# Kernel tuning notes

Hardware: AMD Instinct MI355X
Metric: run time of the kernel (lower is better)

Reference implementation:

```python
import jax, jax.numpy as jnp
import numpy as np

LAM = 0.1       # self.lam
MAX_ITER = 100  # fista_reweighted maxIter
TOL = 1e-5      # convergence tolerance


def creat_dictionary(T, rr, theta):
    # torch creatRealDictionary: row i = [1, rr^i*cos(i*theta), rr^i*sin(i*theta)]
    i = jnp.arange(T, dtype=rr.dtype)[:, None]           # [T,1]
    p = rr[None, :] ** i                                  # [T,P]
    W1 = p * jnp.cos(i * theta[None, :])                  # [T,P]
    W2 = p * jnp.sin(i * theta[None, :])                  # [T,P]
    ones = jnp.ones((T, 1), rr.dtype)
    return jnp.concatenate([ones, W1, W2], axis=1)        # [T, 1+2P]


def fista_reweighted(D, Y, lambd, w):
    # D: [T,K], Y: [N,T,M], w: [N,K,M]
    DtD = D.T @ D                                         # [K,K]
    DtY = jnp.einsum('tk,ntm->nkm', D, Y)                 # [N,K,M]
    # torch.norm(DtD, 2) with no dim = 2-norm of the flattened matrix (Frobenius)
    Linv = 1.0 / jnp.linalg.norm(DtD)
    K = DtD.shape[0]
    A = jnp.eye(K, dtype=D.dtype) - DtD * Linv            # [K,K]
    wl = w * (lambd * Linv)                               # weighted lambda [N,K,M]
    c_minus = DtY * Linv - wl
    c_plus = DtY * Linv + wl
    x0 = jnp.zeros_like(DtY)

    def body(carry, _):
        x_old, y_old, t_old, done = carry
        Ay = jnp.einsum('kj,njm->nkm', A, y_old)
        # shrinkage: max(0, Ay + c-) + min(0, Ay + c+)
        x_new = jnp.maximum(0.0, Ay + c_minus) + jnp.minimum(0.0, Ay + c_plus)
        t_new = (1.0 + jnp.sqrt(1.0 + 4.0 * t_old ** 2)) / 2.0
        tt = (t_old - 1.0) / t_new
        y_new = x_new + tt * (x_new - x_old)
        conv = (jnp.linalg.norm(x_old - x_new) / K) < TOL
        stop = done | conv
        # on convergence torch breaks with x_old = x_new; afterwards freeze state
        x_next = jnp.where(done, x_old, x_new)
        y_next = jnp.where(stop, y_old, y_new)
        t_next = jnp.where(stop, t_old, t_new)
        return (x_next, y_next, t_next, stop), None

    init = (x0, x0, jnp.float32(1.0), jnp.array(False))
    (x, _, _, _), _ = jax.lax.scan(jax.checkpoint(body), init, None, length=MAX_ITER)
    return x


def setup_inputs() -> dict:
    key = jax.random.key(0)
    k1, k2, k3 = jax.random.split(key, 3)
    N, T, M, P = 256, 36, 50, 80
    x = jax.random.normal(k1, (N, T, M), dtype=jnp.float32)
    rr = 0.9 + 0.1 * jax.random.uniform(k2, (P,), dtype=jnp.float32)   # poles near unit circle
    theta = jnp.pi * jax.random.uniform(k3, (P,), dtype=jnp.float32)
    return {"x": x, "rr": rr, "theta": theta, "T": T}


def reference(x, rr, theta, T):
    dic = creat_dictionary(T, rr, theta)                  # [T,K]
    K = dic.shape[1]
    w = jnp.ones((x.shape[0], K, x.shape[2]), x.dtype)    # [N,K,M]
    code = None
    for _ in range(2):                                    # reweighting heuristic, 2 passes
        code = fista_reweighted(dic, x, LAM, w)
        wn = 1.0 / (jnp.abs(code) + 0.01)
        w = wn / jnp.linalg.norm(wn) * K
    reconst = jnp.einsum('tk,nkm->ntm', dic, code)        # [N,T,M]
    return code, dic, reconst
```

## Files before the change

kernel.cpp:

```cpp
#include <hip/hip_runtime.h>
#include <math.h>

#define N_    256
#define T_    36
#define M_    50
#define P_    80
#define K_    161
#define PADK  192
#define KC    24
#define NB    200
#define NT    256
#define LAM_  0.1f
#define MAXIT 100

#define KM_     (K_*M_)
#define TM_     (T_*M_)
#define OUT_DIC 2060800
#define OUT_REC 2066596

#define WS_LINV 0
#define WS_D    64
#define WS_ACC  8192
#define WS_WN   8392
#define WS_BARC 8396
#define WS_BARG 8397

__global__ __launch_bounds__(256) void k_dict(const float* __restrict__ rr,
                                              const float* __restrict__ th,
                                              float* __restrict__ out,
                                              float* __restrict__ ws) {
    __shared__ float Dl[T_*PADK];
    const int tid = threadIdx.x;
    for (int e = tid; e < T_*PADK; e += 256) {
        int t = e / PADK, k = e - (e / PADK) * PADK;
        float v = 0.f;
        if (k == 0) v = 1.f;
        else if (k <= P_)      { float r = rr[k-1];     float a = th[k-1]*(float)t;
                                 v = powf(r, (float)t) * cosf(a); }
        else if (k <= 2*P_)    { float r = rr[k-1-P_];  float a = th[k-1-P_]*(float)t;
                                 v = powf(r, (float)t) * sinf(a); }
        Dl[e] = v;
        ws[WS_D + e] = v;
        if (k < K_) out[OUT_DIC + t*K_ + k] = v;
    }
    __syncthreads();
    float loc = 0.f;
    for (int e = tid; e < T_*T_; e += 256) {
        int t1 = e / T_, t2 = e - (e / T_) * T_;
        float s = 0.f;
        for (int k = 0; k < K_; ++k) s = fmaf(Dl[t1*PADK+k], Dl[t2*PADK+k], s);
        loc = fmaf(s, s, loc);
    }
    #pragma unroll
    for (int mm = 1; mm < 64; mm <<= 1) loc += __shfl_xor(loc, mm);
    __shared__ float rb[4];
    if ((tid & 63) == 0) rb[tid >> 6] = loc;
    __syncthreads();
    if (tid == 0) {
        float tot = rb[0] + rb[1] + rb[2] + rb[3];
        ws[WS_LINV] = 1.0f / sqrtf(tot);
    }
}

__device__ __forceinline__ void grid_barrier(unsigned* cnt, unsigned* gen) {
    __syncthreads();
    if (threadIdx.x == 0) {
        __threadfence();
        unsigned g0 = __hip_atomic_load(gen, __ATOMIC_ACQUIRE, __HIP_MEMORY_SCOPE_AGENT);
        unsigned my = __hip_atomic_fetch_add(cnt, 1u, __ATOMIC_ACQ_REL, __HIP_MEMORY_SCOPE_AGENT);
        if (my == NB - 1u) {
            __hip_atomic_store(cnt, 0u, __ATOMIC_RELAXED, __HIP_MEMORY_SCOPE_AGENT);
            __hip_atomic_fetch_add(gen, 1u, __ATOMIC_RELEASE, __HIP_MEMORY_SCOPE_AGENT);
        } else {
            while (__hip_atomic_load(gen, __ATOMIC_ACQUIRE, __HIP_MEMORY_SCOPE_AGENT) == g0)
                __builtin_amdgcn_s_sleep(1);
        }
        __threadfence();
    }
    __syncthreads();
}

template<int CTRL>
__device__ __forceinline__ float dpp_mov(float v) {
    int p = __builtin_amdgcn_update_dpp(0, __float_as_int(v), CTRL, 0xF, 0xF, true);
    return __int_as_float(p);
}
__device__ __forceinline__ float reduce8(float z) {
    z += dpp_mov<0xB1>(z);
    z += dpp_mov<0x4E>(z);
    z += dpp_mov<0x141>(z);
    return z;
}

__global__ __launch_bounds__(NT, 1) void k_fista(const float* __restrict__ X,
                                                 float* __restrict__ out,
                                                 float* __restrict__ ws) {
    __shared__ __align__(16) float Dl[T_*PADK];
    __shared__ int   sniter;
    __shared__ float sbcast;

    unsigned* wsu = (unsigned*)ws;
    const int tid = threadIdx.x;

    for (int e = tid; e < T_*PADK; e += NT) Dl[e] = ws[WS_D + e];
    const float Linv = ws[WS_LINV];
    __syncthreads();

    const int lane  = tid & 63;
    const int kq    = lane & 7;
    const int gw    = (int)blockIdx.x * (NT/64) + (tid >> 6);
    const int colb  = gw*16 + (lane >> 3)*2;
    const int n0    = colb / M_;
    const int m0    = colb - n0*M_;
    const int n1    = (colb+1) / M_;
    const int m1    = (colb+1) - n1*M_;
    const int kbase = kq * KC;
    const float* Y0 = X + n0*TM_ + m0;
    const float* Y1 = X + n1*TM_ + m1;

    float x[2][KC], y[2][KC], b[2][KC], wl[2][KC];

    #pragma unroll
    for (int j = 0; j < KC; ++j) { b[0][j] = 0.f; b[1][j] = 0.f; }
    #pragma unroll 2
    for (int t = 0; t < T_; ++t) {
        float yv0 = Y0[t*M_], yv1 = Y1[t*M_];
        const float4* dp = (const float4*)(Dl + t*PADK + kbase);
        #pragma unroll
        for (int q = 0; q < KC/4; ++q) {
            float4 d = dp[q];
            b[0][4*q+0] = fmaf(d.x, yv0, b[0][4*q+0]);
            b[0][4*q+1] = fmaf(d.y, yv0, b[0][4*q+1]);
            b[0][4*q+2] = fmaf(d.z, yv0, b[0][4*q+2]);
            b[0][4*q+3] = fmaf(d.w, yv0, b[0][4*q+3]);
            b[1][4*q+0] = fmaf(d.x, yv1, b[1][4*q+0]);
            b[1][4*q+1] = fmaf(d.y, yv1, b[1][4*q+1]);
            b[1][4*q+2] = fmaf(d.z, yv1, b[1][4*q+2]);
            b[1][4*q+3] = fmaf(d.w, yv1, b[1][4*q+3]);
        }
    }
    #pragma unroll
    for (int j = 0; j < KC; ++j) { b[0][j] *= Linv; b[1][j] *= Linv; }

    #pragma unroll
    for (int j = 0; j < KC; ++j) { wl[0][j] = LAM_ * Linv; wl[1][j] = LAM_ * Linv; }

    float tcur = 1.f;

    auto iterate = [&]() -> float {
        float u[2][KC];
        #pragma unroll
        for (int j = 0; j < KC; ++j) { u[0][j] = 0.f; u[1][j] = 0.f; }
        #pragma unroll 2
        for (int t = 0; t < T_; ++t) {
            const float4* dp = (const float4*)(Dl + t*PADK + kbase);
            float4 da[KC/4];
            #pragma unroll
            for (int q = 0; q < KC/4; ++q) da[q] = dp[q];
            float z00=0.f, z01=0.f, z02=0.f, z03=0.f;
            float z10=0.f, z11=0.f, z12=0.f, z13=0.f;
            #pragma unroll
            for (int q = 0; q < KC/4; ++q) {
                z00 = fmaf(da[q].x, y[0][4*q+0], z00);
                z01 = fmaf(da[q].y, y[0][4*q+1], z01);
                z02 = fmaf(da[q].z, y[0][4*q+2], z02);
                z03 = fmaf(da[q].w, y[0][4*q+3], z03);
                z10 = fmaf(da[q].x, y[1][4*q+0], z10);
                z11 = fmaf(da[q].y, y[1][4*q+1], z11);
                z12 = fmaf(da[q].z, y[1][4*q+2], z12);
                z13 = fmaf(da[q].w, y[1][4*q+3], z13);
            }
            float z0 = (z00+z01) + (z02+z03);
            float z1 = (z10+z11) + (z12+z13);
            z0 = reduce8(z0);
            z1 = reduce8(z1);
            #pragma unroll
            for (int q = 0; q < KC/4; ++q) {
                u[0][4*q+0] = fmaf(da[q].x, z0, u[0][4*q+0]);
                u[0][4*q+1] = fmaf(da[q].y, z0, u[0][4*q+1]);
                u[0][4*q+2] = fmaf(da[q].z, z0, u[0][4*q+2]);
                u[0][4*q+3] = fmaf(da[q].w, z0, u[0][4*q+3]);
                u[1][4*q+0] = fmaf(da[q].x, z1, u[1][4*q+0]);
                u[1][4*q+1] = fmaf(da[q].y, z1, u[1][4*q+1]);
                u[1][4*q+2] = fmaf(da[q].z, z1, u[1][4*q+2]);
                u[1][4*q+3] = fmaf(da[q].w, z1, u[1][4*q+3]);
            }
        }
        float t0 = tcur;
        float t1 = 0.5f * (1.f + sqrtf(fmaf(4.f*t0, t0, 1.f)));
        float tt = (t0 - 1.f) / t1;
        tcur = t1;
        float ss = 0.f;
        #pragma unroll
        for (int c = 0; c < 2; ++c) {
            #pragma unroll
            for (int j = 0; j < KC; ++j) {
                float Ay = fmaf(-Linv, u[c][j], y[c][j]);
                float s  = Ay + b[c][j];
                float xn = fmaxf(0.f, s - wl[c][j]) + fminf(0.f, s + wl[c][j]);
                float d  = xn - x[c][j];
                ss    = fmaf(d, d, ss);
                y[c][j] = fmaf(tt, d, xn);
                x[c][j] = xn;
            }
        }
        return ss;
    };

    auto run = [&](int nit, bool record, int accbase) {
        tcur = 1.f;
        #pragma unroll
        for (int j = 0; j < KC; ++j) {
            x[0][j] = 0.f; x[1][j] = 0.f; y[0][j] = 0.f; y[1][j] = 0.f;
        }
        for (int i = 0; i < nit; ++i) {
            float ss = iterate();
            if (record) {
                #pragma unroll
                for (int mm = 1; mm < 64; mm <<= 1) ss += __shfl_xor(ss, mm);
                if (lane == 0) atomicAdd(ws + WS_ACC + accbase + i, ss);
            }
        }
    };

    const float THR2 = (1e-5f * (float)K_) * (1e-5f * (float)K_);

    #pragma unroll 1
    for (int pass = 0; pass < 2; ++pass) {
        run(MAXIT, true, pass*MAXIT);
        grid_barrier(wsu + WS_BARC, wsu + WS_BARG);

        if (tid == 0) sniter = MAXIT + 1;
        __syncthreads();
        if (tid < MAXIT) {
            float a = __hip_atomic_load(ws + WS_ACC + pass*MAXIT + tid,
                                        __ATOMIC_RELAXED, __HIP_MEMORY_SCOPE_AGENT);
            if (a < THR2) atomicMin(&sniter, tid + 1);
        }
        __syncthreads();
        int nit2 = sniter;
        if (nit2 < MAXIT) run(nit2, false, 0);

        if (pass == 0) {
            float loc = 0.f;
            #pragma unroll
            for (int c = 0; c < 2; ++c) {
                #pragma unroll
                for (int j = 0; j < KC; ++j) {
                    float wn = 1.0f / (fabsf(x[c][j]) + 0.01f);
                    wl[c][j] = wn;
                    if (kbase + j < K_) loc = fmaf(wn, wn, loc);
                }
            }
            #pragma unroll
            for (int mm = 1; mm < 64; mm <<= 1) loc += __shfl_xor(loc, mm);
            if (lane == 0) atomicAdd(ws + WS_WN, loc);
            grid_barrier(wsu + WS_BARC, wsu + WS_BARG);
            if (tid == 0)
                sbcast = __hip_atomic_load(ws + WS_WN, __ATOMIC_RELAXED,
                                           __HIP_MEMORY_SCOPE_AGENT);
            __syncthreads();
            float scale = ((float)K_) * (LAM_ * Linv) / sqrtf(sbcast);
            #pragma unroll
            for (int j = 0; j < KC; ++j) { wl[0][j] *= scale; wl[1][j] *= scale; }
        }
    }

    #pragma unroll
    for (int j = 0; j < KC; ++j) {
        int kg = kbase + j;
        if (kg < K_) {
            out[n0*KM_ + kg*M_ + m0] = x[0][j];
            out[n1*KM_ + kg*M_ + m1] = x[1][j];
        }
    }
    #pragma unroll 2
    for (int t = 0; t < T_; ++t) {
        const float4* dp = (const float4*)(Dl + t*PADK + kbase);
        float z00=0.f, z01=0.f, z02=0.f, z03=0.f;
        float z10=0.f, z11=0.f, z12=0.f, z13=0.f;
        #pragma unroll
        for (int q = 0; q < KC/4; ++q) {
            float4 d = dp[q];
            z00 = fmaf(d.x, x[0][4*q+0], z00);
            z01 = fmaf(d.y, x[0][4*q+1], z01);
            z02 = fmaf(d.z, x[0][4*q+2], z02);
            z03 = fmaf(d.w, x[0][4*q+3], z03);
            z10 = fmaf(d.x, x[1][4*q+0], z10);
            z11 = fmaf(d.y, x[1][4*q+1], z11);
            z12 = fmaf(d.z, x[1][4*q+2], z12);
            z13 = fmaf(d.w, x[1][4*q+3], z13);
        }
        float z0 = (z00+z01) + (z02+z03);
        float z1 = (z10+z11) + (z12+z13);
        z0 = reduce8(z0);
        z1 = reduce8(z1);
        if (kq == (t & 7)) {
            out[OUT_REC + n0*TM_ + t*M_ + m0] = z0;
            out[OUT_REC + n1*TM_ + t*M_ + m1] = z1;
        }
    }
}

extern "C" void kernel_launch(void* const* d_in, const int* in_sizes, int n_in,
                              void* d_out, int out_size, void* d_ws, size_t ws_size,
                              hipStream_t stream) {
    const float* X  = (const float*)d_in[0];
    const float* rr = (const float*)d_in[1];
    const float* th = (const float*)d_in[2];
    float* out = (float*)d_out;
    float* ws  = (float*)d_ws;

    hipMemsetAsync((char*)d_ws + WS_ACC*sizeof(float), 0, 4096, stream);
    k_dict<<<dim3(1), dim3(256), 0, stream>>>(rr, th, out, ws);
    k_fista<<<dim3(NB), dim3(NT), 0, stream>>>(X, out, ws);
}
```

Baseline: 1.889 ms.

## Split K across 16 lanes with 512-thread blocks and cache dictionary rows in registers

Each column pair is now handled by 16 lanes holding 12 coefficients each instead of 8 lanes holding 24, with blocks doubled to 512 threads. The DPP reduction gains a fourth step to cover 16 lanes. The first 6 dictionary rows for each lane's slice are preloaded into registers so those rows skip shared-memory loads every iteration. This raises thread-level parallelism and cuts per-thread register state, at the cost of a longer reduction, more lanes touching shared memory, and more cross-block barrier participants.

```diff
diff --git a/kernel.cpp b/kernel.cpp
--- a/kernel.cpp
+++ b/kernel.cpp
@@ -7,9 +7,10 @@
 #define P_    80
 #define K_    161
 #define PADK  192
-#define KC    24
+#define KC    12
+#define NC    6
 #define NB    200
-#define NT    256
+#define NT    512
 #define LAM_  0.1f
 #define MAXIT 100
 
@@ -85,14 +86,15 @@
     int p = __builtin_amdgcn_update_dpp(0, __float_as_int(v), CTRL, 0xF, 0xF, true);
     return __int_as_float(p);
 }
-__device__ __forceinline__ float reduce8(float z) {
+__device__ __forceinline__ float reduce16(float z) {
     z += dpp_mov<0xB1>(z);
     z += dpp_mov<0x4E>(z);
     z += dpp_mov<0x141>(z);
+    z += dpp_mov<0x140>(z);
     return z;
 }
 
-__global__ __launch_bounds__(NT, 1) void k_fista(const float* __restrict__ X,
+__global__ __launch_bounds__(NT, 2) void k_fista(const float* __restrict__ X,
                                                  float* __restrict__ out,
                                                  float* __restrict__ ws) {
     __shared__ __align__(16) float Dl[T_*PADK];
@@ -107,16 +109,23 @@
     __syncthreads();
 
     const int lane  = tid & 63;
-    const int kq    = lane & 7;
+    const int sub   = lane & 15;
     const int gw    = (int)blockIdx.x * (NT/64) + (tid >> 6);
-    const int colb  = gw*16 + (lane >> 3)*2;
+    const int colb  = gw*8 + (lane >> 4)*2;
     const int n0    = colb / M_;
     const int m0    = colb - n0*M_;
     const int n1    = (colb+1) / M_;
     const int m1    = (colb+1) - n1*M_;
-    const int kbase = kq * KC;
+    const int kbase = sub * KC;
     const float* Y0 = X + n0*TM_ + m0;
     const float* Y1 = X + n1*TM_ + m1;
+
+    float4 dc[NC*3];
+    #pragma unroll
+    for (int t = 0; t < NC; ++t) {
+        const float4* dp = (const float4*)(Dl + t*PADK + kbase);
+        dc[t*3+0] = dp[0]; dc[t*3+1] = dp[1]; dc[t*3+2] = dp[2];
+    }
 
     float x[2][KC], y[2][KC], b[2][KC], wl[2][KC];
 
@@ -151,16 +160,13 @@
         float u[2][KC];
         #pragma unroll
         for (int j = 0; j < KC; ++j) { u[0][j] = 0.f; u[1][j] = 0.f; }
-        #pragma unroll 2
-        for (int t = 0; t < T_; ++t) {
-            const float4* dp = (const float4*)(Dl + t*PADK + kbase);
-            float4 da[KC/4];
-            #pragma unroll
-            for (int q = 0; q < KC/4; ++q) da[q] = dp[q];
+
+        auto tbody = [&](float4 d0, float4 d1, float4 d2) {
+            float4 da[3] = {d0, d1, d2};
             float z00=0.f, z01=0.f, z02=0.f, z03=0.f;
             float z10=0.f, z11=0.f, z12=0.f, z13=0.f;
             #pragma unroll
-            for (int q = 0; q < KC/4; ++q) {
+            for (int q = 0; q < 3; ++q) {
                 z00 = fmaf(da[q].x, y[0][4*q+0], z00);
                 z01 = fmaf(da[q].y, y[0][4*q+1], z01);
                 z02 = fmaf(da[q].z, y[0][4*q+2], z02);
@@ -172,10 +178,10 @@
             }
             float z0 = (z00+z01) + (z02+z03);
             float z1 = (z10+z11) + (z12+z13);
-            z0 = reduce8(z0);
-            z1 = reduce8(z1);
-            #pragma unroll
-            for (int q = 0; q < KC/4; ++q) {
+            z0 = reduce16(z0);
+            z1 = reduce16(z1);
+            #pragma unroll
+            for (int q = 0; q < 3; ++q) {
                 u[0][4*q+0] = fmaf(da[q].x, z0, u[0][4*q+0]);
                 u[0][4*q+1] = fmaf(da[q].y, z0, u[0][4*q+1]);
                 u[0][4*q+2] = fmaf(da[q].z, z0, u[0][4*q+2]);
@@ -185,7 +191,17 @@
                 u[1][4*q+2] = fmaf(da[q].z, z1, u[1][4*q+2]);
                 u[1][4*q+3] = fmaf(da[q].w, z1, u[1][4*q+3]);
             }
-        }
+        };
+
+        #pragma unroll
+        for (int t = 0; t < NC; ++t)
+            tbody(dc[t*3+0], dc[t*3+1], dc[t*3+2]);
+        #pragma unroll 2
+        for (int t = NC; t < T_; ++t) {
+            const float4* dp = (const float4*)(Dl + t*PADK + kbase);
+            tbody(dp[0], dp[1], dp[2]);
+        }
+
         float t0 = tcur;
         float t1 = 0.5f * (1.f + sqrtf(fmaf(4.f*t0, t0, 1.f)));
         float tt = (t0 - 1.f) / t1;
@@ -293,9 +309,9 @@
         }
         float z0 = (z00+z01) + (z02+z03);
         float z1 = (z10+z11) + (z12+z13);
-        z0 = reduce8(z0);
-        z1 = reduce8(z1);
-        if (kq == (t & 7)) {
+        z0 = reduce16(z0);
+        z1 = reduce16(z1);
+        if (sub == (t & 15)) {
             out[OUT_REC + n0*TM_ + t*M_ + m0] = z0;
             out[OUT_REC + n1*TM_ + t*M_ + m1] = z1;
         }
```

New measurement: 3.049 ms. 1.61x slower.
